# Performance work log

Measured on AMD Instinct MI355X. Metric: run time of the kernel, lower is better.

Reference implementation:

```python
import jax, jax.numpy as jnp
import numpy as np

B, N, D, R, K = 16384, 20, 64, 3, 64  # batch, triples per sample, embed dim, n_relations, r_dim


def setup_inputs() -> dict:
    key = jax.random.key(0)
    ks = jax.random.split(key, 8)
    # xavier_normal std for [2D, K] matrices: sqrt(2/(2D+K))
    std_w = float(np.sqrt(2.0 / (2 * D + K)))
    std_r = float(np.sqrt(2.0 / (R + K)))
    return {
        "u_emb": jax.random.normal(ks[0], (B, D), dtype=jnp.float32),
        "i_emb": jax.random.normal(ks[1], (B, D), dtype=jnp.float32),
        "a_emb": jax.random.normal(ks[2], (B, N, D), dtype=jnp.float32),
        "o_emb": jax.random.normal(ks[3], (B, N, D), dtype=jnp.float32),
        "s": jax.random.randint(ks[4], (B, N), 0, R, dtype=jnp.int64),
        "w_uir": jax.random.normal(ks[5], (R, 2 * D, K), dtype=jnp.float32) * std_w,
        "w_aor": jax.random.normal(ks[6], (R, 2 * D, K), dtype=jnp.float32) * std_w,
        "r_vec": jax.random.normal(ks[7], (R, K), dtype=jnp.float32) * std_r,
    }


def reference(u_emb, i_emb, a_emb, o_emb, s, w_uir, w_aor, r_vec):
    # transr predictor, bpr loss
    ui_in = jnp.concatenate([u_emb, i_emb], axis=-1)          # [B, 2D]
    ao_in = jnp.concatenate([a_emb, o_emb], axis=-1)          # [B, N, 2D]
    n_rel = w_uir.shape[0]
    ui_emb = jnp.zeros(ao_in.shape[:2] + (w_uir.shape[-1],), dtype=ui_in.dtype)  # [B, N, K]
    ao_emb = jnp.zeros_like(ui_emb)
    for r_idx in range(n_rel):  # small fixed relation count
        m = (s == r_idx)[..., None]                            # [B, N, 1]
        ui_r = ui_in @ w_uir[r_idx] + r_vec[r_idx]             # [B, K]
        ao_r = jnp.einsum("bnd,dk->bnk", ao_in, w_aor[r_idx])  # [B, N, K]
        ui_emb = jnp.where(m, ui_r[:, None, :], ui_emb)
        ao_emb = jnp.where(m, ao_r, ao_emb)
    pred = jnp.sum(ui_emb * ao_emb, axis=-1)                   # [B, N]
    return pred
```

## Files before the change

kernel.cpp:

```cpp
#include <hip/hip_runtime.h>
#include <hip/hip_bf16.h>

#define BB   16384
#define NN   20
#define NREL 3

typedef __attribute__((ext_vector_type(8))) short  short8;
typedef __attribute__((ext_vector_type(4))) float  f32x4;

__device__ __forceinline__ float lo16(unsigned int u) {
    union { unsigned int x; float f; } c; c.x = u << 16; return c.f;
}
__device__ __forceinline__ float hi16(unsigned int u) {
    union { unsigned int x; float f; } c; c.x = u & 0xFFFF0000u; return c.f;
}

__device__ __forceinline__ unsigned short f2bu(float f) {
    union { float f; unsigned int u; } x;
    x.f = f;
    unsigned int r = x.u + 0x7FFFu + ((x.u >> 16) & 1u);
    return (unsigned short)(r >> 16);
}

__global__ __launch_bounds__(256) void k_precompute(
    const float* __restrict__ w_uir,
    const float* __restrict__ w_aor,
    const float* __restrict__ r_vec,
    unsigned short* __restrict__ McatT,
    float* __restrict__ cvec)
{
    int idx = blockIdx.x * 256 + threadIdx.x;
    if (idx < NREL * 128 * 128) {
        int d = idx & 127;
        int e = (idx >> 7) & 127;
        int r = idx >> 14;
        const float4* pu = reinterpret_cast<const float4*>(w_uir + (r * 128 + d) * 64);
        const float4* pa = reinterpret_cast<const float4*>(w_aor + (r * 128 + e) * 64);
        float acc = 0.f;
        #pragma unroll
        for (int k = 0; k < 16; ++k) {
            float4 a = pu[k], b = pa[k];
            acc += a.x * b.x + a.y * b.y + a.z * b.z + a.w * b.w;
        }
        McatT[(r * 128 + e) * 128 + d] = f2bu(acc);
    } else if (idx < NREL * 128 * 128 + NREL * 128) {
        int j = idx - NREL * 128 * 128;
        int r = j >> 7, e = j & 127;
        const float4* pr = reinterpret_cast<const float4*>(r_vec + r * 64);
        const float4* pa = reinterpret_cast<const float4*>(w_aor + (r * 128 + e) * 64);
        float acc = 0.f;
        #pragma unroll
        for (int k = 0; k < 16; ++k) {
            float4 a = pr[k], b = pa[k];
            acc += a.x * b.x + a.y * b.y + a.z * b.z + a.w * b.w;
        }
        cvec[j] = acc;
    }
}

__global__ __launch_bounds__(256) void k_gemm(
    const float* __restrict__ u_emb,
    const float* __restrict__ i_emb,
    const unsigned short* __restrict__ McatT,
    const float* __restrict__ cvec,
    unsigned short* __restrict__ vp)
{
    __shared__ unsigned short Atile[64][136];
    const int t = threadIdx.x;
    const int bm = blockIdx.x & 255;
    const int bn = blockIdx.x >> 8;
    const int Mbase = bm * 64;
    const int Nbase = bn * 64;

    #pragma unroll
    for (int it = 0; it < 8; ++it) {
        int idx  = it * 256 + t;
        int row  = idx >> 5;
        int colg = idx & 31;
        const float* src = (colg < 16)
            ? (u_emb + (Mbase + row) * 64 + colg * 4)
            : (i_emb + (Mbase + row) * 64 + (colg - 16) * 4);
        float4 v = *reinterpret_cast<const float4*>(src);
        ushort4 h;
        h.x = f2bu(v.x); h.y = f2bu(v.y); h.z = f2bu(v.z); h.w = f2bu(v.w);
        *reinterpret_cast<ushort4*>(&Atile[row][colg * 4]) = h;
    }
    __syncthreads();

    const int w    = t >> 6;
    const int lane = t & 63;
    const int lr   = lane & 15;
    const int lk   = (lane >> 4) * 8;

    short8 afrag[4];
    #pragma unroll
    for (int kk = 0; kk < 4; ++kk)
        afrag[kk] = *reinterpret_cast<const short8*>(&Atile[w * 16 + lr][kk * 32 + lk]);

    #pragma unroll
    for (int nt = 0; nt < 4; ++nt) {
        f32x4 acc = {0.f, 0.f, 0.f, 0.f};
        int col = Nbase + nt * 16 + lr;
        #pragma unroll
        for (int kk = 0; kk < 4; ++kk) {
            short8 bfrag = *reinterpret_cast<const short8*>(McatT + col * 128 + kk * 32 + lk);
            acc = __builtin_amdgcn_mfma_f32_16x16x32_bf16(afrag[kk], bfrag, acc, 0, 0, 0);
        }
        float cb = cvec[col];
        #pragma unroll
        for (int reg = 0; reg < 4; ++reg) {
            int grow = Mbase + w * 16 + (lane >> 4) * 4 + reg;
            vp[grow * 384 + col] = f2bu(acc[reg] + cb);
        }
    }
}

#define K3_BLOCKS 1280
#define K3_SWEEP_TRIPS (K3_BLOCKS * 32)
#define K3_SWEEPS 8

__global__ __launch_bounds__(256, 5) void k_pred(
    const float* __restrict__ a_emb,
    const float* __restrict__ o_emb,
    const int* __restrict__ s,
    const unsigned short* __restrict__ vp,
    float* __restrict__ out)
{
    const int lane8 = threadIdx.x & 7;
    const int j8    = lane8 * 8;
    int trip = blockIdx.x * 32 + (threadIdx.x >> 3);

    int sv = s[trip];

    #pragma unroll
    for (int it = 0; it < K3_SWEEPS; ++it) {
        const int trip_next = trip + K3_SWEEP_TRIPS;
        int sv_next = 0;
        if (it + 1 < K3_SWEEPS) sv_next = s[trip_next];

        const float* pa = a_emb + trip * 64 + j8;
        const float* po = o_emb + trip * 64 + j8;
        float4 al = *(const float4*)(pa);
        float4 ah = *(const float4*)(pa + 4);
        float4 ol = *(const float4*)(po);
        float4 oh = *(const float4*)(po + 4);

        unsigned b = (unsigned)trip / NN;
        const unsigned short* vb = vp + (((b * 3u + (unsigned)sv) << 7));
        uint4 wa = *(const uint4*)(vb + j8);
        uint4 wb = *(const uint4*)(vb + 64 + j8);

        float r = al.x * lo16(wa.x) + al.y * hi16(wa.x)
                + al.z * lo16(wa.y) + al.w * hi16(wa.y)
                + ah.x * lo16(wa.z) + ah.y * hi16(wa.z)
                + ah.z * lo16(wa.w) + ah.w * hi16(wa.w)
                + ol.x * lo16(wb.x) + ol.y * hi16(wb.x)
                + ol.z * lo16(wb.y) + ol.w * hi16(wb.y)
                + oh.x * lo16(wb.z) + oh.y * hi16(wb.z)
                + oh.z * lo16(wb.w) + oh.w * hi16(wb.w);

        r += __shfl_xor(r, 4, 64);
        r += __shfl_xor(r, 2, 64);
        r += __shfl_xor(r, 1, 64);
        if (lane8 == 0)
            out[trip] = r;

        sv = sv_next;
        trip = trip_next;
    }
}

extern "C" void kernel_launch(void* const* d_in, const int* in_sizes, int n_in,
                              void* d_out, int out_size, void* d_ws, size_t ws_size,
                              hipStream_t stream) {
    const float* u_emb = (const float*)d_in[0];
    const float* i_emb = (const float*)d_in[1];
    const float* a_emb = (const float*)d_in[2];
    const float* o_emb = (const float*)d_in[3];
    const int*   s     = (const int*)d_in[4];
    const float* w_uir = (const float*)d_in[5];
    const float* w_aor = (const float*)d_in[6];
    const float* r_vec = (const float*)d_in[7];
    float* out = (float*)d_out;

    char* ws = (char*)d_ws;
    unsigned short* McatT = (unsigned short*)ws;
    float*          cvec  = (float*)(ws + 98304);
    unsigned short* vp    = (unsigned short*)(ws + 102400);

    k_precompute<<<194, 256, 0, stream>>>(w_uir, w_aor, r_vec, McatT, cvec);
    k_gemm<<<1536, 256, 0, stream>>>(u_emb, i_emb, McatT, cvec, vp);
    k_pred<<<K3_BLOCKS, 256, 0, stream>>>(a_emb, o_emb, s, vp, out);
}
```

Before: 55.77 us.

## Stage per-batch vp rows in LDS and software-pipeline embedding loads in k_pred

Measured after the change: 53.47 us. -4.1%, faster.

```diff
diff --git a/kernel.cpp b/kernel.cpp
--- a/kernel.cpp
+++ b/kernel.cpp
@@ -115,58 +115,93 @@
     }
 }
 
-#define K3_BLOCKS 1280
-#define K3_SWEEP_TRIPS (K3_BLOCKS * 32)
-#define K3_SWEEPS 8
-
-__global__ __launch_bounds__(256, 5) void k_pred(
+#define K3_BLOCKS 1024
+#define K3_BPB    16
+#define K3_TPB    (K3_BPB * NN)
+#define K3_ITERS  10
+
+__global__ __launch_bounds__(256, 4) void k_pred(
     const float* __restrict__ a_emb,
     const float* __restrict__ o_emb,
     const int* __restrict__ s,
     const unsigned short* __restrict__ vp,
     float* __restrict__ out)
 {
-    const int lane8 = threadIdx.x & 7;
-    const int j8    = lane8 * 8;
-    int trip = blockIdx.x * 32 + (threadIdx.x >> 3);
-
-    int sv = s[trip];
-
-    #pragma unroll
-    for (int it = 0; it < K3_SWEEPS; ++it) {
-        const int trip_next = trip + K3_SWEEP_TRIPS;
-        int sv_next = 0;
-        if (it + 1 < K3_SWEEPS) sv_next = s[trip_next];
-
-        const float* pa = a_emb + trip * 64 + j8;
-        const float* po = o_emb + trip * 64 + j8;
-        float4 al = *(const float4*)(pa);
-        float4 ah = *(const float4*)(pa + 4);
-        float4 ol = *(const float4*)(po);
-        float4 oh = *(const float4*)(po + 4);
-
-        unsigned b = (unsigned)trip / NN;
-        const unsigned short* vb = vp + (((b * 3u + (unsigned)sv) << 7));
-        uint4 wa = *(const uint4*)(vb + j8);
-        uint4 wb = *(const uint4*)(vb + 64 + j8);
-
-        float r = al.x * lo16(wa.x) + al.y * hi16(wa.x)
-                + al.z * lo16(wa.y) + al.w * hi16(wa.y)
-                + ah.x * lo16(wa.z) + ah.y * hi16(wa.z)
-                + ah.z * lo16(wa.w) + ah.w * hi16(wa.w)
-                + ol.x * lo16(wb.x) + ol.y * hi16(wb.x)
-                + ol.z * lo16(wb.y) + ol.w * hi16(wb.y)
-                + oh.x * lo16(wb.z) + oh.y * hi16(wb.z)
-                + oh.z * lo16(wb.w) + oh.w * hi16(wb.w);
+    __shared__ unsigned short vp_lds[K3_BPB * 3 * 128];
+
+    const int tid  = threadIdx.x;
+    const int bid  = blockIdx.x;
+    const int wv   = tid >> 6;
+    const int lane = tid & 63;
+
+    {
+        const char* src_base = (const char*)(vp + (size_t)bid * K3_BPB * 384);
+        #pragma unroll
+        for (int kk = 0; kk < 3; ++kk) {
+            int k = wv * 3 + kk;
+            const char* src = src_base + k * 1024 + lane * 16;
+            char* dst = (char*)vp_lds + k * 1024;
+            __builtin_amdgcn_global_load_lds((const unsigned int*)src,
+                                             (unsigned int*)dst, 16, 0, 0);
+        }
+    }
+    asm volatile("s_waitcnt vmcnt(0)");
+    __syncthreads();
+
+    const int g  = tid >> 3;
+    const int q  = tid & 7;
+    const int j8 = q * 8;
+
+    int trip0 = bid * K3_TPB + g;
+
+    int    sv_c = s[trip0];
+    const float* pa = a_emb + (size_t)trip0 * 64 + j8;
+    const float* po = o_emb + (size_t)trip0 * 64 + j8;
+    float4 a0c = *(const float4*)(pa);
+    float4 a1c = *(const float4*)(pa + 4);
+    float4 o0c = *(const float4*)(po);
+    float4 o1c = *(const float4*)(po + 4);
+
+    #pragma unroll
+    for (int it = 0; it < K3_ITERS; ++it) {
+        const int trip  = trip0 + it * 32;
+        const int ltrip = it * 32 + g;
+
+        int    sv_n = 0;
+        float4 a0n = {}, a1n = {}, o0n = {}, o1n = {};
+        if (it + 1 < K3_ITERS) {
+            const int tn = trip + 32;
+            sv_n = s[tn];
+            const float* pan = a_emb + (size_t)tn * 64 + j8;
+            const float* pon = o_emb + (size_t)tn * 64 + j8;
+            a0n = *(const float4*)(pan);
+            a1n = *(const float4*)(pan + 4);
+            o0n = *(const float4*)(pon);
+            o1n = *(const float4*)(pon + 4);
+        }
+
+        const int bl = ltrip / NN;
+        const unsigned short* vrow = vp_lds + (bl * 3 + sv_c) * 128;
+        uint4 wa = *(const uint4*)(vrow + j8);
+        uint4 wb = *(const uint4*)(vrow + 64 + j8);
+
+        float r = a0c.x * lo16(wa.x) + a0c.y * hi16(wa.x)
+                + a0c.z * lo16(wa.y) + a0c.w * hi16(wa.y)
+                + a1c.x * lo16(wa.z) + a1c.y * hi16(wa.z)
+                + a1c.z * lo16(wa.w) + a1c.w * hi16(wa.w)
+                + o0c.x * lo16(wb.x) + o0c.y * hi16(wb.x)
+                + o0c.z * lo16(wb.y) + o0c.w * hi16(wb.y)
+                + o1c.x * lo16(wb.z) + o1c.y * hi16(wb.z)
+                + o1c.z * lo16(wb.w) + o1c.w * hi16(wb.w);
 
         r += __shfl_xor(r, 4, 64);
         r += __shfl_xor(r, 2, 64);
         r += __shfl_xor(r, 1, 64);
-        if (lane8 == 0)
+        if (q == 0)
             out[trip] = r;
 
-        sv = sv_next;
-        trip = trip_next;
+        sv_c = sv_n;
+        a0c = a0n; a1c = a1n; o0c = o0n; o1c = o1n;
     }
 }
 
```
